# Kernel optimization log

Measured on AMD Instinct MI355X. Metric: run time of the kernel, lower is better.

The kernel has to match this reference:

```python
import jax, jax.numpy as jnp
import numpy as np

N_EMBD = 1024
N_HEAD = 16
HEAD_DIM = N_EMBD // N_HEAD
NEG = -1e9


def setup_inputs() -> dict:
    key = jax.random.key(0)
    ks = jax.random.split(key, 5)
    B, S = 2, 2048
    x = jax.random.normal(ks[0], (B, S, N_EMBD), dtype=jnp.float32)
    # qkv_proj: Linear(n_embd, 3*n_embd) -> weight used as x @ W_qkv (W stored [in, out])
    scale = 1.0 / np.sqrt(N_EMBD)
    W_qkv = jax.random.normal(ks[1], (N_EMBD, 3 * N_EMBD), dtype=jnp.float32) * scale
    b_qkv = jax.random.normal(ks[2], (3 * N_EMBD,), dtype=jnp.float32) * 0.02
    W_out = jax.random.normal(ks[3], (N_EMBD, N_EMBD), dtype=jnp.float32) * scale
    b_out = jax.random.normal(ks[4], (N_EMBD,), dtype=jnp.float32) * 0.02
    return {"x": x, "W_qkv": W_qkv, "b_qkv": b_qkv, "W_out": W_out, "b_out": b_out}


def reference(x, W_qkv, b_qkv, W_out, b_out):
    B, S, E = x.shape
    qkv = x @ W_qkv + b_qkv                      # [B,S,3E]
    q, k, v = jnp.split(qkv, 3, axis=-1)
    # [B,S,E] -> [B,H,S,D]
    def split_heads(t):
        return t.reshape(B, S, N_HEAD, HEAD_DIM).transpose(0, 2, 1, 3)
    q, k, v = split_heads(q), split_heads(k), split_heads(v)
    scores = jnp.einsum("bhqd,bhkd->bhqk", q, k) / jnp.sqrt(jnp.float32(HEAD_DIM))
    causal = jnp.tril(jnp.ones((S, S), dtype=bool))
    scores = jnp.where(causal, scores, NEG)
    attn = jax.nn.softmax(scores, axis=-1)
    out = jnp.einsum("bhqk,bhkd->bhqd", attn, v)  # [B,H,S,D]
    out = out.transpose(0, 2, 1, 3).reshape(B, S, E)
    return out @ W_out + b_out
```

## Files before the change

kernel.cpp:

```cpp
#include <hip/hip_runtime.h>
#include <hip/hip_bf16.h>

#define BATCH 2
#define SEQ   2048
#define EMBD  1024
#define NHEAD 16
#define HDIM  64
#define QKV3  (3 * EMBD)

#define QSCALE 0.18033688011112042f
#define SCLAMP 86.56f

typedef __attribute__((ext_vector_type(8))) __bf16 bf16x8;
typedef __attribute__((ext_vector_type(4))) __bf16 bf16x4;
typedef __attribute__((ext_vector_type(4))) float f32x4;

__device__ __forceinline__ float fast_exp2(float x) {
#if __has_builtin(__builtin_amdgcn_exp2f)
    return __builtin_amdgcn_exp2f(x);
#else
    return exp2f(x);
#endif
}

__global__ __launch_bounds__(256) void prep_fused(
    const float* __restrict__ x,    __bf16* __restrict__ xbf,
    const float* __restrict__ Wqkv, __bf16* __restrict__ Wqkv_t,
    const float* __restrict__ Wout, __bf16* __restrict__ Wout_t)
{
    const int bid = blockIdx.x;
    const int tid = threadIdx.x;

    if (bid < 2048) {
        int i = (bid * 256 + tid) * 8;
        float4 a = *(const float4*)&x[i];
        float4 b = *(const float4*)&x[i + 4];
        bf16x8 o;
        o[0] = (__bf16)a.x; o[1] = (__bf16)a.y; o[2] = (__bf16)a.z; o[3] = (__bf16)a.w;
        o[4] = (__bf16)b.x; o[5] = (__bf16)b.y; o[6] = (__bf16)b.z; o[7] = (__bf16)b.w;
        *(bf16x8*)&xbf[i] = o;
        return;
    }

    __shared__ float t[64][65];
    const float* in; __bf16* out; int N, n0, k0;
    if (bid < 2816) {
        int tile = bid - 2048;
        N = QKV3;
        n0 = (tile % 48) * 64; k0 = (tile / 48) * 64;
        in = Wqkv; out = Wqkv_t;
    } else {
        int tile = bid - 2816;
        N = EMBD;
        n0 = (tile & 15) * 64; k0 = (tile >> 4) * 64;
        in = Wout; out = Wout_t;
    }
    const int K = EMBD;
    #pragma unroll
    for (int p = 0; p < 4; p++) {
        int kr = p * 16 + (tid >> 4);
        int c4 = (tid & 15) * 4;
        float4 v = *(const float4*)&in[(size_t)(k0 + kr) * N + n0 + c4];
        t[kr][c4] = v.x; t[kr][c4 + 1] = v.y; t[kr][c4 + 2] = v.z; t[kr][c4 + 3] = v.w;
    }
    __syncthreads();
    #pragma unroll
    for (int p = 0; p < 4; p++) {
        int nr = p * 16 + (tid >> 4);
        int k4 = (tid & 15) * 4;
        bf16x4 o;
        o[0] = (__bf16)t[k4 + 0][nr];
        o[1] = (__bf16)t[k4 + 1][nr];
        o[2] = (__bf16)t[k4 + 2][nr];
        o[3] = (__bf16)t[k4 + 3][nr];
        *(bf16x4*)&out[(size_t)(n0 + nr) * K + k0 + k4] = o;
    }
}

__global__ __launch_bounds__(512, 4) void gemm_qkv(
    const __bf16* __restrict__ A,
    const __bf16* __restrict__ Bt,
    const float* __restrict__ bias,
    __bf16* __restrict__ C,
    __bf16* __restrict__ vt,
    int M, int N, int K, int nscale)
{
    __shared__ __align__(16) __bf16 As[2 * 128 * 32];
    __shared__ __align__(16) __bf16 Bs[2 * 128 * 32];

    const int tid  = threadIdx.x;
    const int lane = tid & 63;
    const int wave = tid >> 6;
    const int wm = (wave >> 2) * 64;
    const int wn = (wave & 3) * 32;

    const int hw  = (int)(blockIdx.x + gridDim.x * blockIdx.y);
    const int cpx = (int)gridDim.x >> 3;
    const int xcd = hw & 7;
    const int i_  = hw >> 3;
    const int n0 = (xcd * cpx + (i_ % cpx)) * 128;
    const int m0 = (i_ / cpx) * 128;

    const int lm = lane & 15;
    const int kq = lane >> 4;

    f32x4 acc[4][2] = {};

    for (int k0 = 0; k0 < K; k0 += 64) {
        __syncthreads();
        #pragma unroll
        for (int r = 0; r < 2; r++) {
            int flat = r * 512 + tid;
            int kk   = flat >> 9;
            int row  = (flat >> 2) & 127;
            int c4   = flat & 3;
            const char* ga = (const char*)(A + (size_t)(m0 + row) * K
                                             + k0 + kk * 32 + c4 * 8);
            char* la = (char*)As + flat * 16;
            __builtin_amdgcn_global_load_lds(
                (const __attribute__((address_space(1))) void*)ga,
                (__attribute__((address_space(3))) void*)la, 16, 0, 0);
            const char* gb = (const char*)(Bt + (size_t)(n0 + row) * K
                                              + k0 + kk * 32 + c4 * 8);
            char* lb = (char*)Bs + flat * 16;
            __builtin_amdgcn_global_load_lds(
                (const __attribute__((address_space(1))) void*)gb,
                (__attribute__((address_space(3))) void*)lb, 16, 0, 0);
        }
        __syncthreads();

        #pragma unroll
        for (int kk = 0; kk < 2; kk++) {
            bf16x8 af[4], bf[2];
            #pragma unroll
            for (int t = 0; t < 4; t++)
                af[t] = *(const bf16x8*)&As[kk * 4096 + (wm + t * 16 + lm) * 32 + kq * 8];
            #pragma unroll
            for (int t = 0; t < 2; t++)
                bf[t] = *(const bf16x8*)&Bs[kk * 4096 + (wn + t * 16 + lm) * 32 + kq * 8];
            #pragma unroll
            for (int i = 0; i < 4; i++)
                #pragma unroll
                for (int j = 0; j < 2; j++)
                    acc[i][j] = __builtin_amdgcn_mfma_f32_16x16x32_bf16(
                        af[i], bf[j], acc[i][j], 0, 0, 0);
        }
    }

    const int r0 = kq * 4;
    #pragma unroll
    for (int i = 0; i < 4; i++) {
        #pragma unroll
        for (int j = 0; j < 2; j++) {
            int col = n0 + wn + j * 16 + lm;
            float bv = bias[col];
            float sc = (col < nscale) ? QSCALE : 1.0f;
            if (col >= 2 * EMBD) {
                const int hd   = col - 2 * EMBD;
                const int rowb = m0 + wm + i * 16 + r0;
                const int bh   = (rowb >> 11) * 16 + (hd >> 6);
                const int d    = hd & 63;
                const int seq  = rowb & (SEQ - 1);
                bf16x4 o;
                #pragma unroll
                for (int r = 0; r < 4; r++) o[r] = (__bf16)(acc[i][j][r] + bv);
                *(bf16x4*)&vt[((size_t)bh * 64 + d) * SEQ + seq] = o;
            } else {
                #pragma unroll
                for (int r = 0; r < 4; r++) {
                    int row = m0 + wm + i * 16 + r0 + r;
                    C[(size_t)row * N + col] = (__bf16)((acc[i][j][r] + bv) * sc);
                }
            }
        }
    }
}

__global__ __launch_bounds__(256) void gemm_bt_mfma64(
    const __bf16* __restrict__ A,
    const __bf16* __restrict__ Bt,
    const float* __restrict__ bias,
    float* __restrict__ C,
    int M, int N, int K)
{
    __shared__ __align__(16) __bf16 As[2 * 64 * 32];
    __shared__ __align__(16) __bf16 Bs[2 * 64 * 32];

    const int tid  = threadIdx.x;
    const int lane = tid & 63;
    const int wave = tid >> 6;
    const int wm = (wave >> 1) * 32;
    const int wn = (wave & 1) * 32;

    const int hw  = (int)(blockIdx.x + gridDim.x * blockIdx.y);
    const int cpx = (int)gridDim.x >> 3;
    const int xcd = hw & 7;
    const int i_  = hw >> 3;
    const int n0 = (xcd * cpx + (i_ % cpx)) * 64;
    const int m0 = (i_ / cpx) * 64;

    const int lm = lane & 15;
    const int kq = lane >> 4;

    f32x4 acc[2][2] = {};

    for (int k0 = 0; k0 < K; k0 += 64) {
        __syncthreads();
        #pragma unroll
        for (int r = 0; r < 2; r++) {
            int flat = r * 256 + tid;
            int kk   = flat >> 8;
            int row  = (flat >> 2) & 63;
            int c4   = flat & 3;
            const char* ga = (const char*)(A + (size_t)(m0 + row) * K
                                             + k0 + kk * 32 + c4 * 8);
            char* la = (char*)As + flat * 16;
            __builtin_amdgcn_global_load_lds(
                (const __attribute__((address_space(1))) void*)ga,
                (__attribute__((address_space(3))) void*)la, 16, 0, 0);
            const char* gb = (const char*)(Bt + (size_t)(n0 + row) * K
                                              + k0 + kk * 32 + c4 * 8);
            char* lb = (char*)Bs + flat * 16;
            __builtin_amdgcn_global_load_lds(
                (const __attribute__((address_space(1))) void*)gb,
                (__attribute__((address_space(3))) void*)lb, 16, 0, 0);
        }
        __syncthreads();

        #pragma unroll
        for (int kk = 0; kk < 2; kk++) {
            bf16x8 af[2], bf[2];
            #pragma unroll
            for (int t = 0; t < 2; t++) {
                af[t] = *(const bf16x8*)&As[kk * 2048 + (wm + t * 16 + lm) * 32 + kq * 8];
                bf[t] = *(const bf16x8*)&Bs[kk * 2048 + (wn + t * 16 + lm) * 32 + kq * 8];
            }
            #pragma unroll
            for (int i = 0; i < 2; i++)
                #pragma unroll
                for (int j = 0; j < 2; j++)
                    acc[i][j] = __builtin_amdgcn_mfma_f32_16x16x32_bf16(
                        af[i], bf[j], acc[i][j], 0, 0, 0);
        }
    }

    const int r0 = kq * 4;
    #pragma unroll
    for (int i = 0; i < 2; i++) {
        #pragma unroll
        for (int j = 0; j < 2; j++) {
            int col = n0 + wn + j * 16 + lm;
            float bv = bias[col];
            #pragma unroll
            for (int r = 0; r < 4; r++) {
                int row = m0 + wm + i * 16 + r0 + r;
                C[(size_t)row * N + col] = acc[i][j][r] + bv;
            }
        }
    }
}

__global__ __launch_bounds__(256) void attn_kpar_mfma(
    const __bf16* __restrict__ qkv, const __bf16* __restrict__ vt,
    __bf16* __restrict__ attn)
{
    __shared__ __align__(16) char smem[34304];

    const int tid  = threadIdx.x;
    const int wave = tid >> 6;
    const int lane = tid & 63;
    const int quad = lane >> 4;
    const int c    = lane & 15;

    const int bh = blockIdx.x;
    const int b  = bh >> 4;
    const int h  = bh & 15;

    const int y = (int)blockIdx.y;
    const int g = y >> 3, s = y & 7;
    int qblk;
    if      (g == 0) qblk = 31 - s;
    else if (g == 1) qblk = s;
    else if (g == 2) qblk = 23 - s;
    else             qblk = 8 + s;
    const int q0 = qblk * 64;

    const size_t base = (size_t)b * SEQ * QKV3;
    const int hoff = h * HDIM;
    const __bf16* vbase = vt + (size_t)bh * 64 * SEQ;

    bf16x8 aq[4][2];
    #pragma unroll
    for (int qf = 0; qf < 4; qf++) {
        const __bf16* qrow = qkv + base +
            (size_t)(q0 + qf * 16 + c) * QKV3 + hoff + quad * 8;
        aq[qf][0] = *(const bf16x8*)(qrow);
        aq[qf][1] = *(const bf16x8*)(qrow + 32);
    }

    f32x4 acc[4][4] = {};
    float lpart[4] = {};

    char* pbw = smem + wave * 8192;
    const int ntiles = qblk + 1;

    for (int t = wave; t < ntiles; t += 4) {
        const int k0 = t * 64;
        const bool diag = (t == ntiles - 1);

        #pragma unroll
        for (int jj = 0; jj < 4; jj++) {
            const __bf16* krow = qkv + base +
                (size_t)(k0 + jj * 16 + c) * QKV3 + EMBD + hoff + quad * 8;
            bf16x8 bk0 = *(const bf16x8*)(krow);
            bf16x8 bk1 = *(const bf16x8*)(krow + 32);
            const int kb = k0 + jj * 16 + quad * 4;
            const int wb = (jj >> 1) * 1024 + (((jj & 1) * 2 + (quad >> 1))) * 256
                         + c * 16 + (quad & 1) * 8;
            #pragma unroll
            for (int qf = 0; qf < 4; qf++) {
                f32x4 s2 = {};
                s2 = __builtin_amdgcn_mfma_f32_16x16x32_bf16(bk0, aq[qf][0], s2, 0, 0, 0);
                s2 = __builtin_amdgcn_mfma_f32_16x16x32_bf16(bk1, aq[qf][1], s2, 0, 0, 0);
                const int qa = q0 + qf * 16 + c;
                bf16x4 pk;
                #pragma unroll
                for (int r = 0; r < 4; r++) {
                    float p;
                    if (diag && (kb + r > qa)) p = 0.f;
                    else p = fast_exp2(fminf(s2[r], SCLAMP));
                    lpart[qf] += p;
                    pk[r] = (__bf16)p;
                }
                *(bf16x4*)(pbw + qf * 2048 + wb) = pk;
            }
        }

        __builtin_amdgcn_s_setprio(1);
        #pragma unroll
        for (int kc = 0; kc < 2; kc++) {
            bf16x8 ap[4];
            #pragma unroll
            for (int qf = 0; qf < 4; qf++)
                ap[qf] = *(const bf16x8*)(pbw + qf * 2048 + kc * 1024 + lane * 16);
            #pragma unroll
            for (int dd = 0; dd < 4; dd++) {
                const __bf16* vr = vbase + (size_t)(dd * 16 + c) * SEQ
                                 + k0 + kc * 32 + quad * 8;
                bf16x8 bv = *(const bf16x8*)(vr);
                #pragma unroll
                for (int qf = 0; qf < 4; qf++)
                    acc[qf][dd] = __builtin_amdgcn_mfma_f32_16x16x32_bf16(
                        ap[qf], bv, acc[qf][dd], 0, 0, 0);
            }
        }
        __builtin_amdgcn_s_setprio(0);
    }

    #pragma unroll
    for (int qf = 0; qf < 4; qf++) {
        float v = lpart[qf];
        v += __shfl_xor(v, 16);
        v += __shfl_xor(v, 32);
        lpart[qf] = v;
    }

    __syncthreads();

    float* Ored = (float*)smem;
    float* lred = (float*)(smem + 33792);

    if (wave < 2) {
        float* R = Ored + wave * (64 * 66);
        #pragma unroll
        for (int qf = 0; qf < 4; qf++) {
            #pragma unroll
            for (int dd = 0; dd < 4; dd++)
                #pragma unroll
                for (int r = 0; r < 4; r++)
                    R[(qf * 16 + quad * 4 + r) * 66 + dd * 16 + c] = acc[qf][dd][r];
            if (quad == 0) lred[wave * 64 + qf * 16 + c] = lpart[qf];
        }
    }
    __syncthreads();
    if (wave >= 2) {
        float* R = Ored + (wave - 2) * (64 * 66);
        #pragma unroll
        for (int qf = 0; qf < 4; qf++) {
            #pragma unroll
            for (int dd = 0; dd < 4; dd++)
                #pragma unroll
                for (int r = 0; r < 4; r++)
                    R[(qf * 16 + quad * 4 + r) * 66 + dd * 16 + c] += acc[qf][dd][r];
            if (quad == 0) lred[(wave - 2) * 64 + qf * 16 + c] += lpart[qf];
        }
    }
    __syncthreads();

    #pragma unroll
    for (int it = 0; it < 2; it++) {
        const int flat = it * 256 + tid;
        const int row = flat >> 3;
        const int cg  = flat & 7;
        const float l = lred[row] + lred[64 + row];
        const float inv = 1.f / l;
        const float* R0 = Ored + row * 66 + cg * 8;
        const float* R1 = R0 + 64 * 66;
        bf16x8 o;
        #pragma unroll
        for (int i = 0; i < 8; i++) o[i] = (__bf16)((R0[i] + R1[i]) * inv);
        *(bf16x8*)&attn[((size_t)b * SEQ + q0 + row) * EMBD + hoff + cg * 8] = o;
    }
}

extern "C" void kernel_launch(void* const* d_in, const int* in_sizes, int n_in,
                              void* d_out, int out_size, void* d_ws, size_t ws_size,
                              hipStream_t stream)
{
    const float* x     = (const float*)d_in[0];
    const float* W_qkv = (const float*)d_in[1];
    const float* b_qkv = (const float*)d_in[2];
    const float* W_out = (const float*)d_in[3];
    const float* b_out = (const float*)d_in[4];
    float* out = (float*)d_out;

    const int M = BATCH * SEQ;

    __bf16* xbf    = (__bf16*)d_ws;
    __bf16* Wqkv_t = xbf    + (size_t)M * EMBD;
    __bf16* Wout_t = Wqkv_t + (size_t)QKV3 * EMBD;
    __bf16* qkv    = Wout_t + (size_t)EMBD * EMBD;
    __bf16* attn   = qkv    + (size_t)M * QKV3;
    __bf16* vtbuf  = attn   + (size_t)M * EMBD;

    prep_fused<<<3072, 256, 0, stream>>>(x, xbf, W_qkv, Wqkv_t, W_out, Wout_t);

    {
        dim3 grid(QKV3 / 128, M / 128);
        gemm_qkv<<<grid, 512, 0, stream>>>(
            xbf, Wqkv_t, b_qkv, qkv, vtbuf, M, QKV3, EMBD, EMBD);
    }
    {
        dim3 grid(BATCH * NHEAD, SEQ / 64);
        attn_kpar_mfma<<<grid, 256, 0, stream>>>(qkv, vtbuf, attn);
    }
    {
        dim3 grid(EMBD / 64, M / 64);
        gemm_bt_mfma64<<<grid, 256, 0, stream>>>(attn, Wout_t, b_out, out, M, EMBD, EMBD);
    }
}
```

Before: 184.7 us.

## Pair causal query blocks per 8-wave attention block for load balance

The attention kernel now launches 512-thread blocks that each handle two query blocks in sequence, a long one (31-pi) and a short one (pi), so every block does about the same causal work. The key tiles are split across 8 waves instead of 4, the per-wave P staging grows shared memory to 64 KB, and the cross-wave reduction becomes four sync-separated accumulation stages. The goal is to remove tail imbalance from the triangular work distribution and to halve the grid. In exchange it adds barriers, serialises the two phases, and requests launch bounds of (512,4), which may sharply cap registers and cause spills of the 64-float accumulator.

```diff
diff --git a/kernel.cpp b/kernel.cpp
--- a/kernel.cpp
+++ b/kernel.cpp
@@ -260,11 +260,11 @@
     }
 }
 
-__global__ __launch_bounds__(256) void attn_kpar_mfma(
+__global__ __launch_bounds__(512, 4) void attn_kpar_mfma(
     const __bf16* __restrict__ qkv, const __bf16* __restrict__ vt,
     __bf16* __restrict__ attn)
 {
-    __shared__ __align__(16) char smem[34304];
+    __shared__ __align__(16) char smem[65536];
 
     const int tid  = threadIdx.x;
     const int wave = tid >> 6;
@@ -275,141 +275,165 @@
     const int bh = blockIdx.x;
     const int b  = bh >> 4;
     const int h  = bh & 15;
-
-    const int y = (int)blockIdx.y;
-    const int g = y >> 3, s = y & 7;
-    int qblk;
-    if      (g == 0) qblk = 31 - s;
-    else if (g == 1) qblk = s;
-    else if (g == 2) qblk = 23 - s;
-    else             qblk = 8 + s;
-    const int q0 = qblk * 64;
+    const int pi = blockIdx.y;
 
     const size_t base = (size_t)b * SEQ * QKV3;
     const int hoff = h * HDIM;
     const __bf16* vbase = vt + (size_t)bh * 64 * SEQ;
 
-    bf16x8 aq[4][2];
-    #pragma unroll
-    for (int qf = 0; qf < 4; qf++) {
-        const __bf16* qrow = qkv + base +
-            (size_t)(q0 + qf * 16 + c) * QKV3 + hoff + quad * 8;
-        aq[qf][0] = *(const bf16x8*)(qrow);
-        aq[qf][1] = *(const bf16x8*)(qrow + 32);
-    }
-
-    f32x4 acc[4][4] = {};
-    float lpart[4] = {};
-
-    char* pbw = smem + wave * 8192;
-    const int ntiles = qblk + 1;
-
-    for (int t = wave; t < ntiles; t += 4) {
-        const int k0 = t * 64;
-        const bool diag = (t == ntiles - 1);
-
-        #pragma unroll
-        for (int jj = 0; jj < 4; jj++) {
-            const __bf16* krow = qkv + base +
-                (size_t)(k0 + jj * 16 + c) * QKV3 + EMBD + hoff + quad * 8;
-            bf16x8 bk0 = *(const bf16x8*)(krow);
-            bf16x8 bk1 = *(const bf16x8*)(krow + 32);
-            const int kb = k0 + jj * 16 + quad * 4;
-            const int wb = (jj >> 1) * 1024 + (((jj & 1) * 2 + (quad >> 1))) * 256
-                         + c * 16 + (quad & 1) * 8;
-            #pragma unroll
-            for (int qf = 0; qf < 4; qf++) {
-                f32x4 s2 = {};
-                s2 = __builtin_amdgcn_mfma_f32_16x16x32_bf16(bk0, aq[qf][0], s2, 0, 0, 0);
-                s2 = __builtin_amdgcn_mfma_f32_16x16x32_bf16(bk1, aq[qf][1], s2, 0, 0, 0);
-                const int qa = q0 + qf * 16 + c;
-                bf16x4 pk;
-                #pragma unroll
-                for (int r = 0; r < 4; r++) {
-                    float p;
-                    if (diag && (kb + r > qa)) p = 0.f;
-                    else p = fast_exp2(fminf(s2[r], SCLAMP));
-                    lpart[qf] += p;
-                    pk[r] = (__bf16)p;
-                }
-                *(bf16x4*)(pbw + qf * 2048 + wb) = pk;
-            }
-        }
-
-        __builtin_amdgcn_s_setprio(1);
-        #pragma unroll
-        for (int kc = 0; kc < 2; kc++) {
-            bf16x8 ap[4];
-            #pragma unroll
-            for (int qf = 0; qf < 4; qf++)
-                ap[qf] = *(const bf16x8*)(pbw + qf * 2048 + kc * 1024 + lane * 16);
-            #pragma unroll
-            for (int dd = 0; dd < 4; dd++) {
-                const __bf16* vr = vbase + (size_t)(dd * 16 + c) * SEQ
-                                 + k0 + kc * 32 + quad * 8;
-                bf16x8 bv = *(const bf16x8*)(vr);
-                #pragma unroll
-                for (int qf = 0; qf < 4; qf++)
-                    acc[qf][dd] = __builtin_amdgcn_mfma_f32_16x16x32_bf16(
-                        ap[qf], bv, acc[qf][dd], 0, 0, 0);
-            }
-        }
-        __builtin_amdgcn_s_setprio(0);
-    }
-
-    #pragma unroll
-    for (int qf = 0; qf < 4; qf++) {
-        float v = lpart[qf];
-        v += __shfl_xor(v, 16);
-        v += __shfl_xor(v, 32);
-        lpart[qf] = v;
-    }
-
-    __syncthreads();
-
     float* Ored = (float*)smem;
     float* lred = (float*)(smem + 33792);
-
-    if (wave < 2) {
-        float* R = Ored + wave * (64 * 66);
+    char* pbw = smem + wave * 8192;
+
+    #pragma unroll 1
+    for (int ph = 0; ph < 2; ph++) {
+        const int qblk = ph ? pi : (31 - pi);
+        const int q0 = qblk * 64;
+
+        if (ph) __syncthreads();
+
+        bf16x8 aq[4][2];
         #pragma unroll
         for (int qf = 0; qf < 4; qf++) {
-            #pragma unroll
-            for (int dd = 0; dd < 4; dd++)
-                #pragma unroll
-                for (int r = 0; r < 4; r++)
-                    R[(qf * 16 + quad * 4 + r) * 66 + dd * 16 + c] = acc[qf][dd][r];
-            if (quad == 0) lred[wave * 64 + qf * 16 + c] = lpart[qf];
-        }
-    }
-    __syncthreads();
-    if (wave >= 2) {
-        float* R = Ored + (wave - 2) * (64 * 66);
+            const __bf16* qrow = qkv + base +
+                (size_t)(q0 + qf * 16 + c) * QKV3 + hoff + quad * 8;
+            aq[qf][0] = *(const bf16x8*)(qrow);
+            aq[qf][1] = *(const bf16x8*)(qrow + 32);
+        }
+
+        f32x4 acc[4][4] = {};
+        float lpart[4] = {};
+
+        const int ntiles = qblk + 1;
+
+        for (int t = wave; t < ntiles; t += 8) {
+            const int k0 = t * 64;
+            const bool diag = (t == ntiles - 1);
+
+            #pragma unroll
+            for (int jj = 0; jj < 4; jj++) {
+                const __bf16* krow = qkv + base +
+                    (size_t)(k0 + jj * 16 + c) * QKV3 + EMBD + hoff + quad * 8;
+                bf16x8 bk0 = *(const bf16x8*)(krow);
+                bf16x8 bk1 = *(const bf16x8*)(krow + 32);
+                const int kb = k0 + jj * 16 + quad * 4;
+                const int wb = (jj >> 1) * 1024 + (((jj & 1) * 2 + (quad >> 1))) * 256
+                             + c * 16 + (quad & 1) * 8;
+                #pragma unroll
+                for (int qf = 0; qf < 4; qf++) {
+                    f32x4 s2 = {};
+                    s2 = __builtin_amdgcn_mfma_f32_16x16x32_bf16(bk0, aq[qf][0], s2, 0, 0, 0);
+                    s2 = __builtin_amdgcn_mfma_f32_16x16x32_bf16(bk1, aq[qf][1], s2, 0, 0, 0);
+                    const int qa = q0 + qf * 16 + c;
+                    bf16x4 pk;
+                    #pragma unroll
+                    for (int r = 0; r < 4; r++) {
+                        float p;
+                        if (diag && (kb + r > qa)) p = 0.f;
+                        else p = fast_exp2(fminf(s2[r], SCLAMP));
+                        lpart[qf] += p;
+                        pk[r] = (__bf16)p;
+                    }
+                    *(bf16x4*)(pbw + qf * 2048 + wb) = pk;
+                }
+            }
+
+            __builtin_amdgcn_s_setprio(1);
+            #pragma unroll
+            for (int kc = 0; kc < 2; kc++) {
+                bf16x8 ap[4];
+                #pragma unroll
+                for (int qf = 0; qf < 4; qf++)
+                    ap[qf] = *(const bf16x8*)(pbw + qf * 2048 + kc * 1024 + lane * 16);
+                #pragma unroll
+                for (int dd = 0; dd < 4; dd++) {
+                    const __bf16* vr = vbase + (size_t)(dd * 16 + c) * SEQ
+                                     + k0 + kc * 32 + quad * 8;
+                    bf16x8 bv = *(const bf16x8*)(vr);
+                    #pragma unroll
+                    for (int qf = 0; qf < 4; qf++)
+                        acc[qf][dd] = __builtin_amdgcn_mfma_f32_16x16x32_bf16(
+                            ap[qf], bv, acc[qf][dd], 0, 0, 0);
+                }
+            }
+            __builtin_amdgcn_s_setprio(0);
+        }
+
         #pragma unroll
         for (int qf = 0; qf < 4; qf++) {
-            #pragma unroll
-            for (int dd = 0; dd < 4; dd++)
-                #pragma unroll
-                for (int r = 0; r < 4; r++)
-                    R[(qf * 16 + quad * 4 + r) * 66 + dd * 16 + c] += acc[qf][dd][r];
-            if (quad == 0) lred[(wave - 2) * 64 + qf * 16 + c] += lpart[qf];
-        }
-    }
-    __syncthreads();
-
-    #pragma unroll
-    for (int it = 0; it < 2; it++) {
-        const int flat = it * 256 + tid;
-        const int row = flat >> 3;
-        const int cg  = flat & 7;
-        const float l = lred[row] + lred[64 + row];
-        const float inv = 1.f / l;
-        const float* R0 = Ored + row * 66 + cg * 8;
-        const float* R1 = R0 + 64 * 66;
-        bf16x8 o;
-        #pragma unroll
-        for (int i = 0; i < 8; i++) o[i] = (__bf16)((R0[i] + R1[i]) * inv);
-        *(bf16x8*)&attn[((size_t)b * SEQ + q0 + row) * EMBD + hoff + cg * 8] = o;
+            float v = lpart[qf];
+            v += __shfl_xor(v, 16);
+            v += __shfl_xor(v, 32);
+            lpart[qf] = v;
+        }
+
+        __syncthreads();
+
+        if (wave < 2) {
+            float* R = Ored + wave * (64 * 66);
+            #pragma unroll
+            for (int qf = 0; qf < 4; qf++) {
+                #pragma unroll
+                for (int dd = 0; dd < 4; dd++)
+                    #pragma unroll
+                    for (int r = 0; r < 4; r++)
+                        R[(qf * 16 + quad * 4 + r) * 66 + dd * 16 + c] = acc[qf][dd][r];
+                if (quad == 0) lred[wave * 64 + qf * 16 + c] = lpart[qf];
+            }
+        }
+        __syncthreads();
+        if ((wave & 6) == 2) {
+            float* R = Ored + (wave - 2) * (64 * 66);
+            #pragma unroll
+            for (int qf = 0; qf < 4; qf++) {
+                #pragma unroll
+                for (int dd = 0; dd < 4; dd++)
+                    #pragma unroll
+                    for (int r = 0; r < 4; r++)
+                        R[(qf * 16 + quad * 4 + r) * 66 + dd * 16 + c] += acc[qf][dd][r];
+                if (quad == 0) lred[(wave - 2) * 64 + qf * 16 + c] += lpart[qf];
+            }
+        }
+        __syncthreads();
+        if ((wave & 6) == 4) {
+            float* R = Ored + (wave - 4) * (64 * 66);
+            #pragma unroll
+            for (int qf = 0; qf < 4; qf++) {
+                #pragma unroll
+                for (int dd = 0; dd < 4; dd++)
+                    #pragma unroll
+                    for (int r = 0; r < 4; r++)
+                        R[(qf * 16 + quad * 4 + r) * 66 + dd * 16 + c] += acc[qf][dd][r];
+                if (quad == 0) lred[(wave - 4) * 64 + qf * 16 + c] += lpart[qf];
+            }
+        }
+        __syncthreads();
+        if (wave >= 6) {
+            float* R = Ored + (wave - 6) * (64 * 66);
+            #pragma unroll
+            for (int qf = 0; qf < 4; qf++) {
+                #pragma unroll
+                for (int dd = 0; dd < 4; dd++)
+                    #pragma unroll
+                    for (int r = 0; r < 4; r++)
+                        R[(qf * 16 + quad * 4 + r) * 66 + dd * 16 + c] += acc[qf][dd][r];
+                if (quad == 0) lred[(wave - 6) * 64 + qf * 16 + c] += lpart[qf];
+            }
+        }
+        __syncthreads();
+
+        {
+            const int row = tid >> 3;
+            const int cg  = tid & 7;
+            const float l = lred[row] + lred[64 + row];
+            const float inv = 1.f / l;
+            const float* R0 = Ored + row * 66 + cg * 8;
+            const float* R1 = R0 + 64 * 66;
+            bf16x8 o;
+            #pragma unroll
+            for (int i = 0; i < 8; i++) o[i] = (__bf16)((R0[i] + R1[i]) * inv);
+            *(bf16x8*)&attn[((size_t)b * SEQ + q0 + row) * EMBD + hoff + cg * 8] = o;
+        }
     }
 }
 
@@ -441,8 +465,8 @@
             xbf, Wqkv_t, b_qkv, qkv, vtbuf, M, QKV3, EMBD, EMBD);
     }
     {
-        dim3 grid(BATCH * NHEAD, SEQ / 64);
-        attn_kpar_mfma<<<grid, 256, 0, stream>>>(qkv, vtbuf, attn);
+        dim3 grid(BATCH * NHEAD, SEQ / 128);
+        attn_kpar_mfma<<<grid, 512, 0, stream>>>(qkv, vtbuf, attn);
     }
     {
         dim3 grid(EMBD / 64, M / 64);
```

After: 237.5 us. 28.6% more time.
